# Performance work log

Hardware: AMD Instinct MI355X
Metric: run time of the kernel (lower is better)

## Reference

```python
import jax, jax.numpy as jnp
import numpy as np

WS = (7, 7, 7)          # window size (S, H, W)
NUM_HEADS = 6
DIM = 192
B_, NW = 128, 32        # total windows, windows per image (mask dim)
N = WS[0] * WS[1] * WS[2]  # 343 tokens per window


def _relative_position_index():
    # Faithful replica of the torch __init__ logic (incl. indexing='xy' and
    # the 3*W1-1 / 2*W1-1 multipliers).
    cs = np.arange(WS[0]); ch = np.arange(WS[1]); cw = np.arange(WS[2])
    coords = np.stack(np.meshgrid(cs, ch, cw, indexing='xy'))  # (3, Wh, Ws, Ww)
    cf = coords.reshape(3, -1)                                  # (3, N)
    rel = cf[:, :, None] - cf[:, None, :]                       # (3, N, N)
    rel = rel.transpose(1, 2, 0).astype(np.int64)               # (N, N, 3)
    rel[:, :, 0] += WS[0] - 1
    rel[:, :, 1] += WS[1] - 1
    rel[:, :, 2] += WS[2] - 1
    rel[:, :, 0] *= 3 * WS[1] - 1
    rel[:, :, 1] *= 2 * WS[1] - 1
    return rel.sum(-1)                                          # (N, N) int


def setup_inputs() -> dict:
    key = jax.random.key(0)
    ks = jax.random.split(key, 6)
    C = DIM
    x = jax.random.normal(ks[0], (B_, N, C), dtype=jnp.float32)
    mask = jax.random.normal(ks[1], (NW, N, N), dtype=jnp.float32)
    qkv_w = jax.random.normal(ks[2], (3 * C, C), dtype=jnp.float32) * 0.02
    qkv_b = jnp.zeros((3 * C,), dtype=jnp.float32)
    proj_w = jax.random.normal(ks[3], (C, C), dtype=jnp.float32) * 0.02
    proj_b = jnp.zeros((C,), dtype=jnp.float32)
    table_len = (2 * WS[0] - 1) * (2 * WS[1] - 1) * (2 * WS[2] - 1)
    rpb_table = jax.random.normal(ks[4], (table_len, NUM_HEADS), dtype=jnp.float32) * 0.02
    rel_index = jnp.asarray(_relative_position_index(), dtype=jnp.int32)
    return {"x": x, "mask": mask, "qkv_w": qkv_w, "qkv_b": qkv_b,
            "proj_w": proj_w, "proj_b": proj_b, "rpb_table": rpb_table,
            "rel_index": rel_index}


def reference(x, mask, qkv_w, qkv_b, proj_w, proj_b, rpb_table, rel_index):
    B, n, C = x.shape
    H = NUM_HEADS
    hd = C // H
    scale = hd ** (-0.5)
    qkv = x @ qkv_w.T + qkv_b                      # (B, N, 3C)
    qkv = qkv.reshape(B, n, 3, H, hd).transpose(2, 0, 3, 1, 4)  # (3, B, H, N, hd)
    q, k, v = qkv[0] * scale, qkv[1], qkv[2]
    attn = jnp.einsum('bhnd,bhmd->bhnm', q, k)     # (B, H, N, N)
    bias = rpb_table[rel_index.reshape(-1)].reshape(n, n, H)
    attn = attn + bias.transpose(2, 0, 1)[None]    # (B, H, N, N)
    nW = mask.shape[0]
    attn = attn.reshape(B // nW, nW, H, n, n) + mask[None, :, None]
    attn = jax.nn.softmax(attn.reshape(B, H, n, n), axis=-1)
    out = jnp.einsum('bhnm,bhmd->bhnd', attn, v)   # (B, H, N, hd)
    out = out.transpose(0, 2, 1, 3).reshape(B, n, C)
    return out @ proj_w.T + proj_b
```

## Files before the change

kernel.cpp:

```cpp
#include <hip/hip_runtime.h>
#include <hip/hip_fp16.h>
#include <hip/hip_bf16.h>
#include <stdint.h>

#define WN 343
#define NH 6
#define HD 32
#define CD 192
#define NB 128
#define NWM 32
#define BMROW 352
#define BMSLICE (11*16*BMROW)
#define BMKC (16*BMROW)
#define LOG2E 1.4426950408889634f

typedef __attribute__((ext_vector_type(8))) short short8;
typedef __attribute__((ext_vector_type(4))) float f32x4;

__device__ __forceinline__ unsigned short f2bf(float f) {
  union { float f; uint32_t u; } v; v.f = f;
  uint32_t r = v.u + 0x7fffu + ((v.u >> 16) & 1u);
  return (unsigned short)(r >> 16);
}

__device__ __forceinline__ uint32_t pk2bf(float a, float b) {
  __hip_bfloat162 h = __float22bfloat162_rn(make_float2(a, b));
  return *(uint32_t*)&h;
}

__device__ __forceinline__ uint32_t pkh2(float a, float b) {
  __half2 h; h.x = __float2half(a); h.y = __float2half(b);
  return *(uint32_t*)&h;
}

typedef const __attribute__((address_space(1))) unsigned int* gas_ptr;
typedef __attribute__((address_space(3))) unsigned int* las_ptr;
__device__ __forceinline__ void gload16(const unsigned short* g, unsigned short* l) {
  __builtin_amdgcn_global_load_lds((gas_ptr)(const void*)g, (las_ptr)(void*)l, 16, 0, 0);
}

__device__ __forceinline__ void pipe_bar() {
  asm volatile("s_waitcnt vmcnt(0) lgkmcnt(0)" ::: "memory");
  __builtin_amdgcn_sched_barrier(0);
  __builtin_amdgcn_s_barrier();
  __builtin_amdgcn_sched_barrier(0);
}

__global__ __launch_bounds__(256) void prep_kernel(
    const float* __restrict__ wq, const float* __restrict__ wp,
    unsigned short* __restrict__ wqb, unsigned short* __restrict__ wpb,
    const int* __restrict__ rel, const float* __restrict__ rpb,
    const float* __restrict__ mask, uint32_t* __restrict__ bP,
    uint32_t* __restrict__ mP) {
  __shared__ float M[88][33];
  const int bid = blockIdx.x;
  const int tid = threadIdx.x;
  if (bid < 264) {
    const int h = bid / 44;
    const int rem = bid - h * 44;
    const int kc = rem >> 2;
    const int g = rem & 3;
    const int n0 = g * 88;
    const int k0 = kc * 32;
    for (int idx = tid; idx < 88 * 32; idx += 256) {
      int nl = idx >> 5, k = idx & 31;
      int n = n0 + nl;
      int nc = (n < WN) ? n : (WN - 1);
      M[nl][k] = (k0 + k < WN) ? rpb[rel[nc * WN + k0 + k] * NH + h] * LOG2E
                               : -30000.0f;
    }
    __syncthreads();
    uint32_t* outp = bP + (size_t)h * BMSLICE + (size_t)kc * BMKC;
    if (tid < 88) {
      const int nl = tid;
      const int n = n0 + nl;
#pragma unroll
      for (int quad = 0; quad < 4; ++quad) {
        uint4 o;
        o.x = pkh2(M[nl][quad * 8 + 0], M[nl][quad * 8 + 4]);
        o.y = pkh2(M[nl][quad * 8 + 1], M[nl][quad * 8 + 5]);
        o.z = pkh2(M[nl][quad * 8 + 2], M[nl][quad * 8 + 6]);
        o.w = pkh2(M[nl][quad * 8 + 3], M[nl][quad * 8 + 7]);
        *(uint4*)(outp + ((size_t)quad * 352 + n) * 4) = o;
      }
    }
    return;
  }
  int cb = bid - 264;
  if (cb < 352) {
    const int wdx = cb / 11;
    const int kc = cb - wdx * 11;
    const int k0 = kc * 32;
    const float* mw = mask + (size_t)wdx * (WN * WN);
    uint32_t* outp = mP + (size_t)wdx * BMSLICE + (size_t)kc * BMKC;
#pragma unroll
    for (int quad = 0; quad < 4; ++quad) {
      const int q8 = quad * 8;
#pragma unroll
      for (int j = 0; j < 2; ++j) {
        int n = tid + 256 * j;
        if (n < 352) {
          float v[8];
#pragma unroll
          for (int i = 0; i < 8; ++i) {
            int kk = k0 + q8 + i;
            v[i] = (n < WN && kk < WN) ? mw[n * WN + kk] * LOG2E : 0.0f;
          }
          uint4 o;
          o.x = pkh2(v[0], v[4]);
          o.y = pkh2(v[1], v[5]);
          o.z = pkh2(v[2], v[6]);
          o.w = pkh2(v[3], v[7]);
          *(uint4*)(outp + ((size_t)quad * 352 + n) * 4) = o;
        }
      }
    }
    return;
  }
  cb -= 352;
  if (cb < 54) {
    int g = cb * 256 + tid;
    int sk = g / 768; int rem = g - sk * 768;
    int row = rem >> 2; int cc = rem & 3;
    int s = sk / 6; int kt = sk - s * 6;
    int lch = cc ^ ((row >> 1) & 3);
    const float* src = wq + (size_t)(s * 192 + row) * CD + kt * 32 + lch * 8;
    f32x4 a = *(const f32x4*)src;
    f32x4 b = *(const f32x4*)(src + 4);
    union { short8 v8; uint32_t d[4]; } pk;
    pk.d[0] = pk2bf(a[0], a[1]);
    pk.d[1] = pk2bf(a[2], a[3]);
    pk.d[2] = pk2bf(b[0], b[1]);
    pk.d[3] = pk2bf(b[2], b[3]);
    *(short8*)(wqb + (size_t)g * 8) = pk.v8;
    return;
  }
  cb -= 54;
  int g = cb * 256 + tid;
  int kt = g / 768; int rem = g - kt * 768;
  int row = rem >> 2; int cc = rem & 3;
  int lch = cc ^ ((row >> 1) & 3);
  const float* src = wp + (size_t)row * CD + kt * 32 + lch * 8;
  f32x4 a = *(const f32x4*)src;
  f32x4 b = *(const f32x4*)(src + 4);
  union { short8 v8; uint32_t d[4]; } pk;
  pk.d[0] = pk2bf(a[0], a[1]);
  pk.d[1] = pk2bf(a[2], a[3]);
  pk.d[2] = pk2bf(b[0], b[1]);
  pk.d[3] = pk2bf(b[2], b[3]);
  *(short8*)(wpb + (size_t)g * 8) = pk.v8;
}

__global__ __launch_bounds__(256) void qkv_kernel(
    const float* __restrict__ x, const unsigned short* __restrict__ wqb,
    const float* __restrict__ bvec,
    unsigned short* __restrict__ qb, unsigned short* __restrict__ kb,
    unsigned short* __restrict__ vb) {
  __shared__ __align__(16) unsigned short SL[20480];
  const int tid = threadIdx.x;
  const int wave = tid >> 6, lane = tid & 63;
  const int quad = lane >> 4, c = lane & 15;
  const int m0 = blockIdx.x * 128;
  const int s = blockIdx.y;
  const int chk = (quad ^ ((c >> 1) & 3)) * 8;

  f32x4 acc[2][12];
#pragma unroll
  for (int i = 0; i < 2; ++i)
#pragma unroll
    for (int j = 0; j < 12; ++j) acc[i][j] = (f32x4){0.f, 0.f, 0.f, 0.f};

  const size_t wt0 = (size_t)s * 6;
  const int xr = tid >> 2, xch = tid & 3;
  const float* xrow0 = x + (size_t)(m0 + xr) * CD + xch * 8;
  const float* xrow1 = x + (size_t)(m0 + 64 + xr) * CD + xch * 8;
  const int cc0w = (xch ^ ((xr >> 1) & 3)) * 8;
  const int cc1w = (xch ^ (((xr + 64) >> 1) & 3)) * 8;

  f32x4 xa0, xb0, xa1, xb1;
  auto XLOAD = [&](int kt) {
    xa0 = *(const f32x4*)(xrow0 + kt * 32);
    xb0 = *(const f32x4*)(xrow0 + kt * 32 + 4);
    xa1 = *(const f32x4*)(xrow1 + kt * 32);
    xb1 = *(const f32x4*)(xrow1 + kt * 32 + 4);
  };
  auto XWRITE = [&](unsigned short* buf) {
    union { short8 v8; uint32_t d[4]; } pk;
    pk.d[0] = pk2bf(xa0[0], xa0[1]);
    pk.d[1] = pk2bf(xa0[2], xa0[3]);
    pk.d[2] = pk2bf(xb0[0], xb0[1]);
    pk.d[3] = pk2bf(xb0[2], xb0[3]);
    *(short8*)&buf[xr * 32 + cc0w] = pk.v8;
    pk.d[0] = pk2bf(xa1[0], xa1[1]);
    pk.d[1] = pk2bf(xa1[2], xa1[3]);
    pk.d[2] = pk2bf(xb1[0], xb1[1]);
    pk.d[3] = pk2bf(xb1[2], xb1[3]);
    *(short8*)&buf[(64 + xr) * 32 + cc1w] = pk.v8;
  };
  auto WSTAGE = [&](unsigned short* buf, int kt) {
    const unsigned short* gw = wqb + (wt0 + kt) * 6144 + tid * 8;
    unsigned short* lw = buf + 4096 + (size_t)wave * 512;
    gload16(gw, lw);
    gload16(gw + 2048, lw + 2048);
    gload16(gw + 4096, lw + 4096);
  };
  auto COMPUTE = [&](const unsigned short* buf) {
    const unsigned short* XLb = buf;
    const unsigned short* WLb = buf + 4096;
    short8 af0 = *(const short8*)&XLb[(wave * 32 + c) * 32 + chk];
    short8 af1 = *(const short8*)&XLb[(wave * 32 + 16 + c) * 32 + chk];
#pragma unroll
    for (int j = 0; j < 12; ++j) {
      short8 bfr = *(const short8*)&WLb[(j * 16 + c) * 32 + chk];
      acc[0][j] = __builtin_amdgcn_mfma_f32_16x16x32_bf16(af0, bfr, acc[0][j], 0, 0, 0);
      acc[1][j] = __builtin_amdgcn_mfma_f32_16x16x32_bf16(af1, bfr, acc[1][j], 0, 0, 0);
    }
  };

  unsigned short* B0 = SL;
  unsigned short* B1 = SL + 10240;
  XLOAD(0); WSTAGE(B0, 0); XWRITE(B0);
  pipe_bar();
#pragma unroll
  for (int p = 0; p < 3; ++p) {
    XLOAD(2 * p + 1); WSTAGE(B1, 2 * p + 1);
    COMPUTE(B0);
    XWRITE(B1);
    pipe_bar();
    if (p < 2) { XLOAD(2 * p + 2); WSTAGE(B0, 2 * p + 2); }
    COMPUTE(B1);
    if (p < 2) XWRITE(B0);
    pipe_bar();
  }

  const float qscale = 0.25503486f;
  unsigned short* dst = (s == 0) ? qb : ((s == 1) ? kb : vb);
  const float scl = (s == 0) ? qscale : 1.0f;
  const int n0 = s * 192;
  unsigned short* Lh0 = SL;
  unsigned short* Lh1 = SL + 4608;
  for (int hh = 0; hh < 3; ++hh) {
    __syncthreads();
#pragma unroll
    for (int jj = 0; jj < 4; ++jj) {
      int j = hh * 4 + jj;
      int hl = jj >> 1;
      int dd = (jj & 1) * 16 + c;
      float bn = bvec[n0 + j * 16 + c];
      unsigned short* L = hl ? Lh1 : Lh0;
#pragma unroll
      for (int i = 0; i < 2; ++i)
#pragma unroll
        for (int r = 0; r < 4; ++r) {
          int m = wave * 32 + i * 16 + quad * 4 + r;
          L[m * 36 + dd] = f2bf((acc[i][j][r] + bn) * scl);
        }
    }
    __syncthreads();
    const int m = tid & 127;
    const int hl = tid >> 7;
    const int M = m0 + m;
    const int b = M / WN;
    const int tok = M - b * WN;
    const int h = hh * 2 + hl;
    const unsigned short* L = hl ? Lh1 : Lh0;
    unsigned short* drow = dst + (((size_t)b * NH + h) * WN + tok) * HD;
#pragma unroll
    for (int t2 = 0; t2 < 4; ++t2) {
      int d0 = t2 * 8;
      *(short8*)&drow[d0] = *(const short8*)&L[m * 36 + d0];
    }
  }
}

__global__ __launch_bounds__(512) void attn_kernel(
    const unsigned short* __restrict__ qb, const unsigned short* __restrict__ kb,
    const unsigned short* __restrict__ vb, const uint32_t* __restrict__ biasP,
    const uint32_t* __restrict__ maskP, unsigned short* __restrict__ ob) {
  __shared__ __align__(16) unsigned short Ks[352][40];
  __shared__ __align__(16) unsigned short Vt[HD][360];
  const int bid = blockIdx.x;
  const int job = (bid & 7) * 96 + (bid >> 3);
  const int wdx = job / 24;
  const int inner = job - wdx * 24;
  const int h = inner >> 2;
  const int b = (inner & 3) * 32 + wdx;
  const int tid = threadIdx.x;
  const int wave = tid >> 6, lane = tid & 63;
  const int quad = lane >> 4, c = lane & 15;
  const size_t base = ((size_t)b * NH + h) * (WN * HD);
  const unsigned short* q = qb + base;
  const unsigned short* k = kb + base;
  const unsigned short* v = vb + base;
  const uint32_t* bS = biasP + (size_t)h * BMSLICE;
  const uint32_t* mS = maskP + (size_t)wdx * BMSLICE;

  for (int t = tid; t < WN * 4; t += 512) {
    int r = t >> 2, ch = t & 3;
    int kk = r & 31;
    int row = (r & ~31) + 16 * ((kk >> 2) & 1) + 4 * (kk >> 3) + (kk & 3);
    *(short8*)&Ks[row][ch * 8] = *(const short8*)(k + r * HD + ch * 8);
  }
  for (int t = tid; t < 9 * 32; t += 512) {
    int kg = WN + (t >> 5);
    int kk = kg & 31;
    int row = (kg & ~31) + 16 * ((kk >> 2) & 1) + 4 * (kk >> 3) + (kk & 3);
    Ks[row][t & 31] = 0;
  }
  for (int t = tid; t < WN; t += 512) {
#pragma unroll
    for (int ch = 0; ch < 4; ++ch) {
      short8 vv = *(const short8*)(v + t * HD + ch * 8);
#pragma unroll
      for (int j = 0; j < 8; ++j) Vt[ch * 8 + j][t] = vv[j];
    }
  }
  for (int t = tid; t < 9 * 32; t += 512) {
    Vt[t & 31][WN + (t >> 5)] = 0;
  }
  __syncthreads();

  union { short8 v8; uint32_t d[4]; } on;
  on.d[0] = on.d[1] = on.d[2] = on.d[3] = 0x3F803F80u;

  for (int qt = wave; qt < 22; qt += 8) {
    const int q0 = qt * 16;
    int qr = q0 + c; if (qr > WN - 1) qr = WN - 1;
    const short8 qf = *(const short8*)(q + qr * HD + quad * 8);
    const uint32_t* bPtr = bS + ((size_t)quad * 352 + q0 + c) * 4;
    const uint32_t* mPtr = mS + ((size_t)quad * 352 + q0 + c) * 4;

    f32x4 o0 = (f32x4){0.f, 0.f, 0.f, 0.f};
    f32x4 o1 = (f32x4){0.f, 0.f, 0.f, 0.f};
    f32x4 accl = (f32x4){0.f, 0.f, 0.f, 0.f};
    uint4 bw = *(const uint4*)bPtr;
    uint4 mw = *(const uint4*)mPtr;
#pragma unroll 1
    for (int kc = 0; kc < 11; ++kc) {
      bPtr += BMKC; mPtr += BMKC;
      uint4 bwN = *(const uint4*)bPtr;
      uint4 mwN = *(const uint4*)mPtr;
      f32x4 cc0, cc1;
      {
        __half2 s2; float2 f;
        s2 = __hadd2(*(__half2*)&bw.x, *(__half2*)&mw.x);
        f = __half22float2(s2); cc0[0] = f.x; cc1[0] = f.y;
        s2 = __hadd2(*(__half2*)&bw.y, *(__half2*)&mw.y);
        f = __half22float2(s2); cc0[1] = f.x; cc1[1] = f.y;
        s2 = __hadd2(*(__half2*)&bw.z, *(__half2*)&mw.z);
        f = __half22float2(s2); cc0[2] = f.x; cc1[2] = f.y;
        s2 = __hadd2(*(__half2*)&bw.w, *(__half2*)&mw.w);
        f = __half22float2(s2); cc0[3] = f.x; cc1[3] = f.y;
      }
      const int k0 = kc * 32;
      short8 kf0 = *(const short8*)&Ks[k0 + c][quad * 8];
      short8 kf1 = *(const short8*)&Ks[k0 + 16 + c][quad * 8];
      __builtin_amdgcn_s_setprio(1);
      f32x4 s0 = __builtin_amdgcn_mfma_f32_16x16x32_bf16(kf0, qf, cc0, 0, 0, 0);
      f32x4 s1 = __builtin_amdgcn_mfma_f32_16x16x32_bf16(kf1, qf, cc1, 0, 0, 0);
      __builtin_amdgcn_s_setprio(0);
      float p0 = __builtin_amdgcn_exp2f(s0[0]), p1 = __builtin_amdgcn_exp2f(s0[1]);
      float p2 = __builtin_amdgcn_exp2f(s0[2]), p3 = __builtin_amdgcn_exp2f(s0[3]);
      float p4 = __builtin_amdgcn_exp2f(s1[0]), p5 = __builtin_amdgcn_exp2f(s1[1]);
      float p6 = __builtin_amdgcn_exp2f(s1[2]), p7 = __builtin_amdgcn_exp2f(s1[3]);
      union { short8 v8; uint32_t d[4]; } pf;
      pf.d[0] = pk2bf(p0, p1);
      pf.d[1] = pk2bf(p2, p3);
      pf.d[2] = pk2bf(p4, p5);
      pf.d[3] = pk2bf(p6, p7);
      short8 vf0 = *(const short8*)&Vt[c][k0 + quad * 8];
      short8 vf1 = *(const short8*)&Vt[16 + c][k0 + quad * 8];
      __builtin_amdgcn_s_setprio(1);
      o0 = __builtin_amdgcn_mfma_f32_16x16x32_bf16(pf.v8, vf0, o0, 0, 0, 0);
      o1 = __builtin_amdgcn_mfma_f32_16x16x32_bf16(pf.v8, vf1, o1, 0, 0, 0);
      accl = __builtin_amdgcn_mfma_f32_16x16x32_bf16(pf.v8, on.v8, accl, 0, 0, 0);
      __builtin_amdgcn_s_setprio(0);
      bw = bwN; mw = mwN;
    }

#pragma unroll
    for (int r = 0; r < 4; ++r) {
      int n = q0 + quad * 4 + r;
      if (n < WN) {
        float inv = 1.0f / accl[r];
        int M = b * WN + n;
        int rloc = M & 127;
        int xr2 = (rloc >> 1) & 3;
        size_t base2 = (((size_t)(M >> 7) * 6 + h) << 12) + rloc * 32;
        ob[base2 + (((c >> 3) ^ xr2) << 3) + (c & 7)] = f2bf(o0[r] * inv);
        ob[base2 + ((((c >> 3) | 2) ^ xr2) << 3) + (c & 7)] = f2bf(o1[r] * inv);
      }
    }
  }
}

__global__ __launch_bounds__(256) void proj_kernel(
    const unsigned short* __restrict__ obp, const unsigned short* __restrict__ wpb,
    const float* __restrict__ bvec, float* __restrict__ out) {
  __shared__ __align__(16) unsigned short SL[16384];
  const int tid = threadIdx.x;
  const int wave = tid >> 6, lane = tid & 63;
  const int quad = lane >> 4, c = lane & 15;
  const int m0 = blockIdx.x * 64;
  const int mb = blockIdx.x >> 1;
  const int r0 = (blockIdx.x & 1) * 64;
  const int chk = (quad ^ ((c >> 1) & 3)) * 8;

  f32x4 acc[12];
#pragma unroll
  for (int j = 0; j < 12; ++j) acc[j] = (f32x4){0.f, 0.f, 0.f, 0.f};

  auto STAGE = [&](unsigned short* buf, int kt) {
    const unsigned short* gx =
        obp + (((size_t)mb * 6 + kt) << 12) + r0 * 32 + tid * 8;
    const unsigned short* gw = wpb + (size_t)kt * 6144 + tid * 8;
    unsigned short* lx = buf + (size_t)wave * 512;
    unsigned short* lw = buf + 2048 + (size_t)wave * 512;
    gload16(gx, lx);
    gload16(gw, lw);
    gload16(gw + 2048, lw + 2048);
    gload16(gw + 4096, lw + 4096);
  };
  auto COMPUTE = [&](const unsigned short* buf) {
    const unsigned short* XLb = buf;
    const unsigned short* WLb = buf + 2048;
    short8 af = *(const short8*)&XLb[(wave * 16 + c) * 32 + chk];
#pragma unroll
    for (int j = 0; j < 12; ++j) {
      short8 bfr = *(const short8*)&WLb[(j * 16 + c) * 32 + chk];
      acc[j] = __builtin_amdgcn_mfma_f32_16x16x32_bf16(af, bfr, acc[j], 0, 0, 0);
    }
  };

  unsigned short* B0 = SL;
  unsigned short* B1 = SL + 8192;
  STAGE(B0, 0);
  pipe_bar();
#pragma unroll
  for (int p = 0; p < 3; ++p) {
    STAGE(B1, 2 * p + 1);
    COMPUTE(B0);
    pipe_bar();
    if (p < 2) STAGE(B0, 2 * p + 2);
    COMPUTE(B1);
    pipe_bar();
  }

#pragma unroll
  for (int j = 0; j < 12; ++j) {
    int col = j * 16 + c;
    float bn = bvec[col];
#pragma unroll
    for (int r = 0; r < 4; ++r) {
      int m = m0 + wave * 16 + quad * 4 + r;
      out[(size_t)m * CD + col] = acc[j][r] + bn;
    }
  }
}

extern "C" void kernel_launch(void* const* d_in, const int* in_sizes, int n_in,
                              void* d_out, int out_size, void* d_ws, size_t ws_size,
                              hipStream_t stream) {
  const float* x      = (const float*)d_in[0];
  const float* mask   = (const float*)d_in[1];
  const float* qkv_w  = (const float*)d_in[2];
  const float* qkv_b  = (const float*)d_in[3];
  const float* proj_w = (const float*)d_in[4];
  const float* proj_b = (const float*)d_in[5];
  const float* rpb    = (const float*)d_in[6];
  const int*   rel    = (const int*)d_in[7];
  float* out = (float*)d_out;

  char* ws = (char*)d_ws;
  uint32_t* biasP = (uint32_t*)ws;
  size_t off = 1486848;
  uint32_t* maskP = (uint32_t*)(ws + off); off += 7929856;
  unsigned short* qb = (unsigned short*)(ws + off); off += 16859136;
  unsigned short* kb = (unsigned short*)(ws + off); off += 16859136;
  unsigned short* vb = (unsigned short*)(ws + off); off += 16859136;
  unsigned short* wqb = (unsigned short*)(ws + off); off += 221184;
  unsigned short* wpb = (unsigned short*)(ws + off); off += 73728;
  unsigned short* obuf = (unsigned short*)(ws + off); off += 16859136;

  hipLaunchKernelGGL(prep_kernel, dim3(264 + 352 + 54 + 18), dim3(256),
                     0, stream,
                     qkv_w, proj_w, wqb, wpb, rel, rpb, mask, biasP, maskP);
  hipLaunchKernelGGL(qkv_kernel, dim3(343, 3), dim3(256), 0, stream,
                     x, wqb, qkv_b, qb, kb, vb);
  hipLaunchKernelGGL(attn_kernel, dim3(NH * NB), dim3(512), 0, stream,
                     qb, kb, vb, biasP, maskP, obuf);
  hipLaunchKernelGGL(proj_kernel, dim3(686), dim3(256), 0, stream,
                     obuf, wpb, proj_b, out);
}
```

Measured before the change: 213.7 us.

## Keep x tile resident in LDS and compute Q, K, V in one block

The QKV projection kernel now launches 343 blocks instead of 343x3. Each block loads and converts its 128-row x tile to bf16 once into LDS (all six k-chunks), then loops over the three Q/K/V weight slices, double-buffering only the weight tiles. This removes the threefold re-read and re-conversion of x from global memory. In exchange it cuts the grid parallelism by three, raises LDS use per block (about 74 KB), and serialises the three outputs within a block, which may lower occupancy and latency hiding.

```diff
diff --git a/kernel.cpp b/kernel.cpp
--- a/kernel.cpp
+++ b/kernel.cpp
@@ -13,6 +13,7 @@
 #define BMSLICE (11*16*BMROW)
 #define BMKC (16*BMROW)
 #define LOG2E 1.4426950408889634f
+#define XTS 4112
 
 typedef __attribute__((ext_vector_type(8))) short short8;
 typedef __attribute__((ext_vector_type(4))) float f32x4;
@@ -156,119 +157,108 @@
     const float* __restrict__ bvec,
     unsigned short* __restrict__ qb, unsigned short* __restrict__ kb,
     unsigned short* __restrict__ vb) {
-  __shared__ __align__(16) unsigned short SL[20480];
+  __shared__ __align__(16) unsigned short SL[6 * XTS + 2 * 6144];
+  unsigned short* B0 = SL + 6 * XTS;
+  unsigned short* B1 = B0 + 6144;
   const int tid = threadIdx.x;
   const int wave = tid >> 6, lane = tid & 63;
   const int quad = lane >> 4, c = lane & 15;
   const int m0 = blockIdx.x * 128;
-  const int s = blockIdx.y;
   const int chk = (quad ^ ((c >> 1) & 3)) * 8;
 
-  f32x4 acc[2][12];
-#pragma unroll
-  for (int i = 0; i < 2; ++i)
-#pragma unroll
-    for (int j = 0; j < 12; ++j) acc[i][j] = (f32x4){0.f, 0.f, 0.f, 0.f};
-
-  const size_t wt0 = (size_t)s * 6;
-  const int xr = tid >> 2, xch = tid & 3;
-  const float* xrow0 = x + (size_t)(m0 + xr) * CD + xch * 8;
-  const float* xrow1 = x + (size_t)(m0 + 64 + xr) * CD + xch * 8;
-  const int cc0w = (xch ^ ((xr >> 1) & 3)) * 8;
-  const int cc1w = (xch ^ (((xr + 64) >> 1) & 3)) * 8;
-
-  f32x4 xa0, xb0, xa1, xb1;
-  auto XLOAD = [&](int kt) {
-    xa0 = *(const f32x4*)(xrow0 + kt * 32);
-    xb0 = *(const f32x4*)(xrow0 + kt * 32 + 4);
-    xa1 = *(const f32x4*)(xrow1 + kt * 32);
-    xb1 = *(const f32x4*)(xrow1 + kt * 32 + 4);
-  };
-  auto XWRITE = [&](unsigned short* buf) {
-    union { short8 v8; uint32_t d[4]; } pk;
-    pk.d[0] = pk2bf(xa0[0], xa0[1]);
-    pk.d[1] = pk2bf(xa0[2], xa0[3]);
-    pk.d[2] = pk2bf(xb0[0], xb0[1]);
-    pk.d[3] = pk2bf(xb0[2], xb0[3]);
-    *(short8*)&buf[xr * 32 + cc0w] = pk.v8;
-    pk.d[0] = pk2bf(xa1[0], xa1[1]);
-    pk.d[1] = pk2bf(xa1[2], xa1[3]);
-    pk.d[2] = pk2bf(xb1[0], xb1[1]);
-    pk.d[3] = pk2bf(xb1[2], xb1[3]);
-    *(short8*)&buf[(64 + xr) * 32 + cc1w] = pk.v8;
-  };
-  auto WSTAGE = [&](unsigned short* buf, int kt) {
-    const unsigned short* gw = wqb + (wt0 + kt) * 6144 + tid * 8;
-    unsigned short* lw = buf + 4096 + (size_t)wave * 512;
+  auto WSTAGE = [&](unsigned short* buf, int s, int kt) {
+    const unsigned short* gw = wqb + ((size_t)s * 6 + kt) * 6144 + tid * 8;
+    unsigned short* lw = buf + (size_t)wave * 512;
     gload16(gw, lw);
     gload16(gw + 2048, lw + 2048);
     gload16(gw + 4096, lw + 4096);
   };
-  auto COMPUTE = [&](const unsigned short* buf) {
-    const unsigned short* XLb = buf;
-    const unsigned short* WLb = buf + 4096;
-    short8 af0 = *(const short8*)&XLb[(wave * 32 + c) * 32 + chk];
-    short8 af1 = *(const short8*)&XLb[(wave * 32 + 16 + c) * 32 + chk];
-#pragma unroll
-    for (int j = 0; j < 12; ++j) {
-      short8 bfr = *(const short8*)&WLb[(j * 16 + c) * 32 + chk];
-      acc[0][j] = __builtin_amdgcn_mfma_f32_16x16x32_bf16(af0, bfr, acc[0][j], 0, 0, 0);
-      acc[1][j] = __builtin_amdgcn_mfma_f32_16x16x32_bf16(af1, bfr, acc[1][j], 0, 0, 0);
-    }
-  };
-
-  unsigned short* B0 = SL;
-  unsigned short* B1 = SL + 10240;
-  XLOAD(0); WSTAGE(B0, 0); XWRITE(B0);
+
+  WSTAGE(B0, 0, 0);
+#pragma unroll
+  for (int it = 0; it < 12; ++it) {
+    int u = tid + 256 * it;
+    int lrow = u / 24, c24 = u - lrow * 24;
+    int kt = c24 >> 2, j = c24 & 3;
+    const float* src = x + (size_t)(m0 + lrow) * CD + kt * 32 + j * 8;
+    f32x4 a = *(const f32x4*)src;
+    f32x4 b = *(const f32x4*)(src + 4);
+    union { short8 v8; uint32_t d[4]; } pk;
+    pk.d[0] = pk2bf(a[0], a[1]);
+    pk.d[1] = pk2bf(a[2], a[3]);
+    pk.d[2] = pk2bf(b[0], b[1]);
+    pk.d[3] = pk2bf(b[2], b[3]);
+    int cw = (j ^ ((lrow >> 1) & 3)) * 8;
+    *(short8*)&SL[kt * XTS + lrow * 32 + cw] = pk.v8;
+  }
   pipe_bar();
-#pragma unroll
-  for (int p = 0; p < 3; ++p) {
-    XLOAD(2 * p + 1); WSTAGE(B1, 2 * p + 1);
-    COMPUTE(B0);
-    XWRITE(B1);
-    pipe_bar();
-    if (p < 2) { XLOAD(2 * p + 2); WSTAGE(B0, 2 * p + 2); }
-    COMPUTE(B1);
-    if (p < 2) XWRITE(B0);
-    pipe_bar();
-  }
 
   const float qscale = 0.25503486f;
-  unsigned short* dst = (s == 0) ? qb : ((s == 1) ? kb : vb);
-  const float scl = (s == 0) ? qscale : 1.0f;
-  const int n0 = s * 192;
-  unsigned short* Lh0 = SL;
-  unsigned short* Lh1 = SL + 4608;
-  for (int hh = 0; hh < 3; ++hh) {
-    __syncthreads();
-#pragma unroll
-    for (int jj = 0; jj < 4; ++jj) {
-      int j = hh * 4 + jj;
-      int hl = jj >> 1;
-      int dd = (jj & 1) * 16 + c;
-      float bn = bvec[n0 + j * 16 + c];
-      unsigned short* L = hl ? Lh1 : Lh0;
-#pragma unroll
-      for (int i = 0; i < 2; ++i)
-#pragma unroll
-        for (int r = 0; r < 4; ++r) {
-          int m = wave * 32 + i * 16 + quad * 4 + r;
-          L[m * 36 + dd] = f2bf((acc[i][j][r] + bn) * scl);
-        }
-    }
-    __syncthreads();
-    const int m = tid & 127;
-    const int hl = tid >> 7;
-    const int M = m0 + m;
-    const int b = M / WN;
-    const int tok = M - b * WN;
-    const int h = hh * 2 + hl;
-    const unsigned short* L = hl ? Lh1 : Lh0;
-    unsigned short* drow = dst + (((size_t)b * NH + h) * WN + tok) * HD;
-#pragma unroll
-    for (int t2 = 0; t2 < 4; ++t2) {
-      int d0 = t2 * 8;
-      *(short8*)&drow[d0] = *(const short8*)&L[m * 36 + d0];
+  f32x4 acc[2][12];
+  unsigned short* Lh0 = B0;
+  unsigned short* Lh1 = B0 + 4608;
+
+  for (int s = 0; s < 3; ++s) {
+#pragma unroll
+    for (int i = 0; i < 2; ++i)
+#pragma unroll
+      for (int j = 0; j < 12; ++j) acc[i][j] = (f32x4){0.f, 0.f, 0.f, 0.f};
+
+    for (int kt = 0; kt < 6; ++kt) {
+      unsigned short* cur = (kt & 1) ? B1 : B0;
+      unsigned short* nxt = (kt & 1) ? B0 : B1;
+      if (kt < 5) WSTAGE(nxt, s, kt + 1);
+      const unsigned short* XLb = SL + kt * XTS;
+      short8 af0 = *(const short8*)&XLb[(wave * 32 + c) * 32 + chk];
+      short8 af1 = *(const short8*)&XLb[(wave * 32 + 16 + c) * 32 + chk];
+#pragma unroll
+      for (int j = 0; j < 12; ++j) {
+        short8 bfr = *(const short8*)&cur[(j * 16 + c) * 32 + chk];
+        acc[0][j] = __builtin_amdgcn_mfma_f32_16x16x32_bf16(af0, bfr, acc[0][j], 0, 0, 0);
+        acc[1][j] = __builtin_amdgcn_mfma_f32_16x16x32_bf16(af1, bfr, acc[1][j], 0, 0, 0);
+      }
+      pipe_bar();
+    }
+
+    unsigned short* dst = (s == 0) ? qb : ((s == 1) ? kb : vb);
+    const float scl = (s == 0) ? qscale : 1.0f;
+    const int n0 = s * 192;
+    for (int hh = 0; hh < 3; ++hh) {
+      __syncthreads();
+#pragma unroll
+      for (int jj = 0; jj < 4; ++jj) {
+        int j = hh * 4 + jj;
+        int hl = jj >> 1;
+        int dd = (jj & 1) * 16 + c;
+        float bn = bvec[n0 + j * 16 + c];
+        unsigned short* L = hl ? Lh1 : Lh0;
+#pragma unroll
+        for (int i = 0; i < 2; ++i)
+#pragma unroll
+          for (int r = 0; r < 4; ++r) {
+            int m = wave * 32 + i * 16 + quad * 4 + r;
+            L[m * 36 + dd] = f2bf((acc[i][j][r] + bn) * scl);
+          }
+      }
+      __syncthreads();
+      const int m = tid & 127;
+      const int hl = tid >> 7;
+      const int M = m0 + m;
+      const int b = M / WN;
+      const int tok = M - b * WN;
+      const int h = hh * 2 + hl;
+      const unsigned short* L = hl ? Lh1 : Lh0;
+      unsigned short* drow = dst + (((size_t)b * NH + h) * WN + tok) * HD;
+#pragma unroll
+      for (int t2 = 0; t2 < 4; ++t2) {
+        int d0 = t2 * 8;
+        *(short8*)&drow[d0] = *(const short8*)&L[m * 36 + d0];
+      }
+    }
+    if (s < 2) {
+      __syncthreads();
+      WSTAGE(B0, s + 1, 0);
+      pipe_bar();
     }
   }
 }
@@ -485,7 +475,7 @@
   hipLaunchKernelGGL(prep_kernel, dim3(264 + 352 + 54 + 18), dim3(256),
                      0, stream,
                      qkv_w, proj_w, wqb, wpb, rel, rpb, mask, biasP, maskP);
-  hipLaunchKernelGGL(qkv_kernel, dim3(343, 3), dim3(256), 0, stream,
+  hipLaunchKernelGGL(qkv_kernel, dim3(343), dim3(256), 0, stream,
                      x, wqb, qkv_b, qb, kb, vb);
   hipLaunchKernelGGL(attn_kernel, dim3(NH * NB), dim3(512), 0, stream,
                      qb, kb, vb, biasP, maskP, obuf);
```

New measurement: 204.2 us. 4.5% less time.
